# Optimization experiments

Measured on AMD Instinct MI355X. Metric: run time of the kernel, lower is better.

Reference implementation:

```python
import jax, jax.numpy as jnp
import numpy as np

B, T, D = 2, 2048, 1024
H, DK, DV, M = 4, 256, 256, 256  # heads, head_k_dim, head_v_dim, num_slots
GATE_NORM = 8.0
SCALE = 1.0
EPS = 1e-5


def setup_inputs() -> dict:
    key = jax.random.key(0)
    ks = jax.random.split(key, 7)
    w = lambda k, shp: jax.random.normal(k, shp, dtype=jnp.float32) * 0.02
    return {
        "hidden_states": jax.random.normal(ks[0], (B, T, D), dtype=jnp.float32),
        "Wq": w(ks[1], (H * DK, D)),   # q_proj
        "Wk": w(ks[2], (H * DK, D)),   # k_proj (num_kv_groups == 1)
        "Wv": w(ks[3], (H * DV, D)),   # v_proj
        "Wf": w(ks[4], (H * M, D)),    # f_proj (num_kv_heads * num_slots)
        "g_w": jnp.ones((H * DV,), dtype=jnp.float32),  # RMSNorm weight
        "Wo": w(ks[5], (D, H * DV)),   # o_proj
    }


def _gsa(q, k, v, s, f, scale):
    """Two-pass GLA recurrence (GSA). All inputs time-major [T,B,H,*]."""
    Bb, Hh = q.shape[1], q.shape[2]
    gk = jnp.exp(f)  # [T,B,H,M] decay in (0,1)

    # Pass 1: Hk_t = Hk_{t-1} * g_t (over slot dim) + k_t (x) s_t ; ok_t = q_t @ Hk_t
    def step1(S, inp):
        qt, kt, st, gt = inp
        S = S * gt[..., None, :] + kt[..., :, None] * st[..., None, :]
        return S, jnp.einsum('bhk,bhkm->bhm', qt * scale, S)

    S0k = jnp.zeros((Bb, Hh, DK, M), q.dtype)
    _, ok = jax.lax.scan(step1, S0k, (q, k, s, gk))

    qv = jax.nn.softmax(ok, axis=-1)  # [T,B,H,M]

    # Pass 2: Hv_t = Hv_{t-1} * g_t (over slot dim) + s_t (x) v_t ; o_t = qv_t @ Hv_t
    def step2(S, inp):
        qt, st, vt, gt = inp
        S = S * gt[..., :, None] + st[..., :, None] * vt[..., None, :]
        return S, jnp.einsum('bhm,bhmv->bhv', qt, S)

    S0v = jnp.zeros((Bb, Hh, M, DV), q.dtype)
    _, ov = jax.lax.scan(step2, S0v, (qv, s, v, gk))
    return ov  # [T,B,H,DV]


def reference(hidden_states, Wq, Wk, Wv, Wf, g_w, Wo):
    Bb, Tt, Dd = hidden_states.shape
    q = (hidden_states @ Wq.T).reshape(Bb, Tt, H, DK)
    k = (hidden_states @ Wk.T).reshape(Bb, Tt, H, DK)
    v = (hidden_states @ Wv.T).reshape(Bb, Tt, H, DV)
    f = (hidden_states @ Wf.T).reshape(Bb, Tt, H, M)

    q = jax.nn.silu(q)            # swish feature map
    k = jax.nn.silu(k)
    v = jax.nn.silu(v)
    f = jax.nn.log_sigmoid(f) / GATE_NORM   # forget-gate log decay
    s = 1.0 - jnp.exp(f)                     # slot write strength

    tm = lambda x: jnp.transpose(x, (1, 0, 2, 3))  # -> time-major
    ov = _gsa(tm(q), tm(k), tm(v), tm(s), tm(f), SCALE)
    o = jnp.transpose(ov, (1, 0, 2, 3)).reshape(Bb, Tt, H * DV)

    # rms_norm_linear(silu(o), g_norm.weight, None, Wo, None), norm in fp32
    o = jax.nn.silu(o)
    o32 = o.astype(jnp.float32)
    rms = o32 * jax.lax.rsqrt(jnp.mean(o32 * o32, axis=-1, keepdims=True) + EPS)
    return (rms * g_w).astype(hidden_states.dtype) @ Wo.T
```

## Files before the change

### kernel.cpp

```cpp
#include <hip/hip_runtime.h>
#include <math.h>

#define TLEN 2048
#define NROWS 4096
#define CHK 64
#define NCHK 32

typedef unsigned short u16;
typedef unsigned int u32;
typedef __attribute__((ext_vector_type(8))) short bf16x8;
typedef __attribute__((ext_vector_type(4))) float f32x4;

#define MFMA(a, b, c) __builtin_amdgcn_mfma_f32_16x16x32_bf16(a, b, c, 0, 0, 0)

__device__ __forceinline__ float bf2f(u16 u) {
    u32 v = ((u32)u) << 16; float f; __builtin_memcpy(&f, &v, 4); return f;
}
__device__ __forceinline__ u16 f2bf(float x) {
    u32 u; __builtin_memcpy(&u, &x, 4);
    u += 0x7FFFu + ((u >> 16) & 1u);
    return (u16)(u >> 16);
}
__device__ __forceinline__ u32 pack2bf(float a, float b) {
    return (u32)f2bf(a) | ((u32)f2bf(b) << 16);
}
__device__ __forceinline__ float bflo(u32 u) { return bf2f((u16)(u & 0xFFFFu)); }
__device__ __forceinline__ float bfhi(u32 u) { return bf2f((u16)(u >> 16)); }
__device__ __forceinline__ float siluf(float x) { return x / (1.f + expf(-x)); }

__global__ void gsa_detect(const u32* __restrict__ gw, int* __restrict__ flag) {
    *flag = (gw[0] == 0x3F803F80u) ? 1 : 0;
}

__global__ __launch_bounds__(256) void gsa_tobf16(const void* __restrict__ src,
        u16* __restrict__ dst, int n8, const int* __restrict__ flag) {
    int i = blockIdx.x * 256 + threadIdx.x;
    if (i >= n8) return;
    if (*flag) {
        ((uint4*)dst)[i] = ((const uint4*)src)[i];
    } else {
        float4 a = ((const float4*)src)[2 * i];
        float4 b = ((const float4*)src)[2 * i + 1];
        uint4 o;
        o.x = pack2bf(a.x, a.y); o.y = pack2bf(a.z, a.w);
        o.z = pack2bf(b.x, b.y); o.w = pack2bf(b.z, b.w);
        ((uint4*)dst)[i] = o;
    }
}

__global__ __launch_bounds__(256) void gsa_emit(const float* __restrict__ src,
        void* __restrict__ dst, int n4, const int* __restrict__ flag) {
    int i = blockIdx.x * 256 + threadIdx.x;
    if (i >= n4) return;
    float4 v = ((const float4*)src)[i];
    if (*flag) {
        uint2 u; u.x = pack2bf(v.x, v.y); u.y = pack2bf(v.z, v.w);
        ((uint2*)dst)[i] = u;
    } else {
        ((float4*)dst)[i] = v;
    }
}

#define GLOAD_LDS16(g, l) \
    __builtin_amdgcn_global_load_lds((const __attribute__((address_space(1))) void*)(g), \
                                     (__attribute__((address_space(3))) void*)(l), 16, 0, 0)

__global__ __launch_bounds__(256) void gsa_gemm_mfma(const u16* __restrict__ A,
        const u16* __restrict__ W0, const u16* __restrict__ W1,
        const u16* __restrict__ W2, const u16* __restrict__ W3,
        void* __restrict__ O0, void* __restrict__ O1,
        void* __restrict__ O2, void* __restrict__ O3, int actpack, int obfmask) {
    __shared__ u16 As[128 * 32];
    __shared__ u16 Bs[128 * 32];
    int tid = threadIdx.x;
    int sel = blockIdx.x >> 3;
    int ntile = blockIdx.x & 7;
    int mtile = blockIdx.y;
    const u16* W = (sel == 0) ? W0 : (sel == 1) ? W1 : (sel == 2) ? W2 : W3;
    void* Out    = (sel == 0) ? O0 : (sel == 1) ? O1 : (sel == 2) ? O2 : O3;
    int act = (actpack >> (sel * 8)) & 0xff;
    int obf = (obfmask >> sel) & 1;
    int w = tid >> 6, lane = tid & 63;
    int wm = w >> 1, wn = w & 1;
    int m0 = wm * 64, n0 = wn * 64;
    int srow = w * 32 + (lane >> 2);
    int scol = (lane & 3) * 8;
    const u16* Abase = A + (size_t)(mtile * 128 + srow) * 1024 + scol;
    const u16* Wbase = W + (size_t)(ntile * 128 + srow) * 1024 + scol;
    u16* AsDst0 = &As[(w * 32) * 32];
    u16* BsDst0 = &Bs[(w * 32) * 32];
    f32x4 acc[4][4];
    #pragma unroll
    for (int i = 0; i < 4; i++)
        #pragma unroll
        for (int j = 0; j < 4; j++) acc[i][j] = (f32x4){0.f, 0.f, 0.f, 0.f};
    int frow = lane & 15, fq = lane >> 4;
    for (int k0 = 0; k0 < 1024; k0 += 32) {
        __syncthreads();
        GLOAD_LDS16(Abase + k0, AsDst0);
        GLOAD_LDS16(Abase + k0 + (size_t)16 * 1024, AsDst0 + 16 * 32);
        GLOAD_LDS16(Wbase + k0, BsDst0);
        GLOAD_LDS16(Wbase + k0 + (size_t)16 * 1024, BsDst0 + 16 * 32);
        __syncthreads();
        bf16x8 af[4], bfv[4];
        #pragma unroll
        for (int mt = 0; mt < 4; mt++)
            af[mt] = *(const bf16x8*)&As[(m0 + mt * 16 + frow) * 32 + fq * 8];
        #pragma unroll
        for (int nt = 0; nt < 4; nt++)
            bfv[nt] = *(const bf16x8*)&Bs[(n0 + nt * 16 + frow) * 32 + fq * 8];
        #pragma unroll
        for (int mt = 0; mt < 4; mt++)
            #pragma unroll
            for (int nt = 0; nt < 4; nt++)
                acc[mt][nt] = MFMA(af[mt], bfv[nt], acc[mt][nt]);
    }
    #pragma unroll
    for (int mt = 0; mt < 4; mt++) {
        #pragma unroll
        for (int nt = 0; nt < 4; nt++) {
            #pragma unroll
            for (int r = 0; r < 4; r++) {
                float x = acc[mt][nt][r];
                int grow = mtile * 128 + m0 + mt * 16 + fq * 4 + r;
                int gcol = ntile * 128 + n0 + nt * 16 + frow;
                float val;
                if (act == 0) val = siluf(x);
                else if (act == 1) {
                    float ls = (x >= 0.f) ? -log1pf(expf(-x)) : (x - log1pf(expf(x)));
                    val = expf(0.125f * ls);
                } else val = x;
                size_t o = (size_t)grow * 1024 + gcol;
                if (obf) ((u16*)Out)[o] = f2bf(val);
                else     ((float*)Out)[o] = val;
            }
        }
    }
}

template<int P>
__global__ __launch_bounds__(256) void gsa_p_local(const u16* __restrict__ Xb,
        const float* __restrict__ GKp, u16* __restrict__ Sb, float* __restrict__ ECb) {
    __shared__ u16 Xt[256 * 72];
    __shared__ u16 Wt[256 * 72];
    int tid = threadIdx.x;
    int bh = blockIdx.x & 7, c = blockIdx.x >> 3;
    int b = bh >> 2, h = bh & 3, t0 = c * CHK;
    size_t gbase = ((size_t)(b * TLEN + t0)) * 1024 + h * 256;
    {
        const u16* xp = Xb + gbase + tid;
        #pragma unroll
        for (int t8 = 0; t8 < 8; t8++) {
            bf16x8 v;
            #pragma unroll
            for (int j = 0; j < 8; j++) v[j] = (short)xp[(size_t)(t8 * 8 + j) * 1024];
            *(bf16x8*)&Xt[tid * 72 + t8 * 8] = v;
        }
    }
    {
        float g[CHK], f[CHK];
        const float* gp = GKp + gbase + tid;
        #pragma unroll
        for (int t = 0; t < CHK; t++) g[t] = gp[(size_t)t * 1024];
        float phiC = 0.f;
        #pragma unroll
        for (int t = 0; t < CHK; t++) { f[t] = __logf(g[t]); phiC += f[t]; }
        if (P == 1) ECb[(bh * NCHK + c) * 256 + tid] = __expf(phiC);
        float phi = 0.f;
        #pragma unroll
        for (int t8 = 0; t8 < 8; t8++) {
            bf16x8 v;
            #pragma unroll
            for (int j = 0; j < 8; j++) {
                phi += f[t8 * 8 + j];
                v[j] = (short)f2bf((1.f - g[t8 * 8 + j]) * __expf(phiC - phi));
            }
            *(bf16x8*)&Wt[tid * 72 + t8 * 8] = v;
        }
    }
    __syncthreads();
    int w = tid >> 6, lane = tid & 63, frow = lane & 15, fq = lane >> 4;
    const u16* Arows = (P == 1) ? Wt : Xt;
    const u16* Brows = (P == 1) ? Xt : Wt;
    bf16x8 afr[4][2];
    #pragma unroll
    for (int it = 0; it < 4; it++)
        #pragma unroll
        for (int ks = 0; ks < 2; ks++)
            afr[it][ks] = *(const bf16x8*)&Arows[(w * 64 + it * 16 + frow) * 72 + ks * 32 + fq * 8];
    u16* Sp = Sb + (size_t)(bh * NCHK + c) * 65536;
    for (int jt = 0; jt < 16; jt++) {
        f32x4 ac[4];
        #pragma unroll
        for (int it = 0; it < 4; it++) ac[it] = (f32x4){0.f, 0.f, 0.f, 0.f};
        #pragma unroll
        for (int ks = 0; ks < 2; ks++) {
            bf16x8 bfr = *(const bf16x8*)&Brows[(jt * 16 + frow) * 72 + ks * 32 + fq * 8];
            #pragma unroll
            for (int it = 0; it < 4; it++) ac[it] = MFMA(afr[it][ks], bfr, ac[it]);
        }
        #pragma unroll
        for (int it = 0; it < 4; it++)
            #pragma unroll
            for (int r = 0; r < 4; r++)
                Sp[(size_t)(w * 64 + it * 16 + fq * 4 + r) * 256 + jt * 16 + frow]
                    = f2bf(ac[it][r]);
    }
}

__global__ __launch_bounds__(256) void gsa_scan1(u16* __restrict__ Sb,
        const float* __restrict__ ECb) {
    int bh = blockIdx.x & 7, part = blockIdx.x >> 3;
    int lin = part * 1024 + threadIdx.x * 4;
    int m = lin >> 8, k = lin & 255;
    u16* Sp = Sb + (size_t)bh * NCHK * 65536 + m * 256 + k;
    const float* Ep = ECb + bh * NCHK * 256 + m;
    float s0 = 0.f, s1 = 0.f, s2 = 0.f, s3 = 0.f;
    for (int c = 0; c < NCHK; c++) {
        uint2 d = *(uint2*)(Sp + (size_t)c * 65536);
        float ec = Ep[c * 256];
        uint2 o; o.x = pack2bf(s0, s1); o.y = pack2bf(s2, s3);
        *(uint2*)(Sp + (size_t)c * 65536) = o;
        s0 = fmaf(ec, s0, bflo(d.x)); s1 = fmaf(ec, s1, bfhi(d.x));
        s2 = fmaf(ec, s2, bflo(d.y)); s3 = fmaf(ec, s3, bfhi(d.y));
    }
}
__global__ __launch_bounds__(256) void gsa_scan2(u16* __restrict__ Sb,
        const float* __restrict__ ECb) {
    int bh = blockIdx.x & 7, part = blockIdx.x >> 3;
    int lin = part * 1024 + threadIdx.x * 4;
    int v = lin >> 8, m = lin & 255;
    u16* Sp = Sb + (size_t)bh * NCHK * 65536 + v * 256 + m;
    const float* Ep = ECb + bh * NCHK * 256 + m;
    float s0 = 0.f, s1 = 0.f, s2 = 0.f, s3 = 0.f;
    for (int c = 0; c < NCHK; c++) {
        uint2 d = *(uint2*)(Sp + (size_t)c * 65536);
        float4 e = *(const float4*)(Ep + c * 256);
        uint2 o; o.x = pack2bf(s0, s1); o.y = pack2bf(s2, s3);
        *(uint2*)(Sp + (size_t)c * 65536) = o;
        s0 = fmaf(e.x, s0, bflo(d.x)); s1 = fmaf(e.y, s1, bfhi(d.x));
        s2 = fmaf(e.z, s2, bflo(d.y)); s3 = fmaf(e.w, s3, bfhi(d.y));
    }
}

__global__ __launch_bounds__(256) void gsa_p1_out(const u16* __restrict__ Qb,
        const u16* __restrict__ Kb, const float* __restrict__ GKp,
        const u16* __restrict__ Sb, float* __restrict__ OK) {
    __shared__ u16 Qs[64 * 264];
    __shared__ float Asc[64 * 68];
    __shared__ float Gs[64 * 260];
    int tid = threadIdx.x;
    int bh = blockIdx.x & 7, c = blockIdx.x >> 3;
    int b = bh >> 2, h = bh & 3, t0 = c * CHK;
    size_t gbase = ((size_t)(b * TLEN + t0)) * 1024 + h * 256;
    #pragma unroll
    for (int j = 0; j < 8; j++) {
        int lin = j * 256 + tid;
        int t = lin >> 5, kg = (lin & 31) * 8;
        *(bf16x8*)&Qs[t * 264 + kg] = *(const bf16x8*)(Qb + gbase + (size_t)t * 1024 + kg);
    }
    __syncthreads();
    int w = tid >> 6, lane = tid & 63, frow = lane & 15, fq = lane >> 4;
    {
        const u16* Kg = Kb + gbase;
        #pragma unroll
        for (int tt = 0; tt < 4; tt++) {
            f32x4 ac = (f32x4){0.f, 0.f, 0.f, 0.f};
            #pragma unroll
            for (int ks = 0; ks < 8; ks++) {
                bf16x8 a = *(const bf16x8*)&Qs[(w * 16 + frow) * 264 + ks * 32 + fq * 8];
                bf16x8 bb = *(const bf16x8*)(Kg + (size_t)(tt * 16 + frow) * 1024 + ks * 32 + fq * 8);
                ac = MFMA(a, bb, ac);
            }
            #pragma unroll
            for (int r = 0; r < 4; r++) {
                int t = w * 16 + fq * 4 + r, tau = tt * 16 + frow;
                Asc[t * 68 + tau] = (tau <= t) ? ac[r] : 0.f;
            }
        }
    }
    {
        const u16* Sg = Sb + (size_t)(bh * NCHK + c) * 65536;
        f32x4 gac[4][4];
        #pragma unroll
        for (int tt = 0; tt < 4; tt++)
            #pragma unroll
            for (int mt = 0; mt < 4; mt++) gac[tt][mt] = (f32x4){0.f, 0.f, 0.f, 0.f};
        for (int ks = 0; ks < 8; ks++) {
            bf16x8 bfr[4], afr[4];
            #pragma unroll
            for (int mt = 0; mt < 4; mt++)
                bfr[mt] = *(const bf16x8*)(Sg + (size_t)(w * 64 + mt * 16 + frow) * 256 + ks * 32 + fq * 8);
            #pragma unroll
            for (int tt = 0; tt < 4; tt++)
                afr[tt] = *(const bf16x8*)&Qs[(tt * 16 + frow) * 264 + ks * 32 + fq * 8];
            #pragma unroll
            for (int tt = 0; tt < 4; tt++)
                #pragma unroll
                for (int mt = 0; mt < 4; mt++)
                    gac[tt][mt] = MFMA(afr[tt], bfr[mt], gac[tt][mt]);
        }
        #pragma unroll
        for (int tt = 0; tt < 4; tt++)
            #pragma unroll
            for (int mt = 0; mt < 4; mt++)
                #pragma unroll
                for (int r = 0; r < 4; r++)
                    Gs[(tt * 16 + fq * 4 + r) * 260 + w * 64 + mt * 16 + frow] = gac[tt][mt][r];
    }
    __syncthreads();
    float E[CHK], U[CHK];
    {
        float g[CHK];
        const float* gp = GKp + gbase + tid;
        #pragma unroll
        for (int t = 0; t < CHK; t++) g[t] = gp[(size_t)t * 1024];
        float phi = 0.f;
        #pragma unroll
        for (int t = 0; t < CHK; t++) {
            float f = __logf(g[t]); phi += f;
            E[t] = __expf(phi);
            U[t] = (1.f - g[t]) * __expf(-phi);
        }
    }
    float* okp = OK + gbase + tid;
    #pragma unroll
    for (int t = 0; t < CHK; t++) {
        float acc = 0.f;
        const int NG = (t < 32) ? 8 : 16;
        #pragma unroll
        for (int j = 0; j < NG; j++) {
            float4 a4 = *(const float4*)&Asc[t * 68 + j * 4];
            acc = fmaf(a4.x, U[4 * j + 0], acc);
            acc = fmaf(a4.y, U[4 * j + 1], acc);
            acc = fmaf(a4.z, U[4 * j + 2], acc);
            acc = fmaf(a4.w, U[4 * j + 3], acc);
        }
        okp[(size_t)t * 1024] = E[t] * (Gs[t * 260 + tid] + acc);
    }
}

__global__ __launch_bounds__(256) void gsa_softmax(float* __restrict__ x) {
    int row = blockIdx.x * 4 + (threadIdx.x >> 6);
    int lane = threadIdx.x & 63;
    float* p = x + (size_t)row * 256 + lane * 4;
    float4 v = *(float4*)p;
    float mx = fmaxf(fmaxf(v.x, v.y), fmaxf(v.z, v.w));
    #pragma unroll
    for (int off = 32; off; off >>= 1) mx = fmaxf(mx, __shfl_xor(mx, off));
    v.x = expf(v.x - mx); v.y = expf(v.y - mx);
    v.z = expf(v.z - mx); v.w = expf(v.w - mx);
    float sm = v.x + v.y + v.z + v.w;
    #pragma unroll
    for (int off = 32; off; off >>= 1) sm += __shfl_xor(sm, off);
    float inv = 1.f / sm;
    v.x *= inv; v.y *= inv; v.z *= inv; v.w *= inv;
    *(float4*)p = v;
}

__global__ __launch_bounds__(256) void gsa_p2_out(const float* __restrict__ QV,
        const u16* __restrict__ Vb, const float* __restrict__ GKp,
        const u16* __restrict__ Sb, float* __restrict__ OV) {
    __shared__ u16 qe[64 * 264];
    __shared__ u16 Us[64 * 264];
    __shared__ float Bsc[64 * 68];
    __shared__ float Gs[64 * 260];
    int tid = threadIdx.x;
    int bh = blockIdx.x & 7, c = blockIdx.x >> 3;
    int b = bh >> 2, h = bh & 3, t0 = c * CHK;
    size_t gbase = ((size_t)(b * TLEN + t0)) * 1024 + h * 256;
    {
        float g[CHK], qv[CHK];
        const float* gp = GKp + gbase + tid;
        const float* qp = QV + gbase + tid;
        #pragma unroll
        for (int t = 0; t < CHK; t++) g[t] = gp[(size_t)t * 1024];
        #pragma unroll
        for (int t = 0; t < CHK; t++) qv[t] = qp[(size_t)t * 1024];
        float phi = 0.f;
        #pragma unroll
        for (int t = 0; t < CHK; t++) {
            float f = __logf(g[t]); phi += f;
            float E = __expf(phi);
            qe[t * 264 + tid] = f2bf(qv[t] * E);
            Us[t * 264 + tid] = f2bf((1.f - g[t]) * __expf(-phi));
        }
    }
    __syncthreads();
    int w = tid >> 6, lane = tid & 63, frow = lane & 15, fq = lane >> 4;
    {
        const u16* Sg = Sb + (size_t)(bh * NCHK + c) * 65536;
        f32x4 gac[4][4];
        #pragma unroll
        for (int tt = 0; tt < 4; tt++)
            #pragma unroll
            for (int vt = 0; vt < 4; vt++) gac[tt][vt] = (f32x4){0.f, 0.f, 0.f, 0.f};
        for (int ks = 0; ks < 8; ks++) {
            bf16x8 bfr[4], afr[4];
            #pragma unroll
            for (int vt = 0; vt < 4; vt++)
                bfr[vt] = *(const bf16x8*)(Sg + (size_t)(w * 64 + vt * 16 + frow) * 256 + ks * 32 + fq * 8);
            #pragma unroll
            for (int tt = 0; tt < 4; tt++)
                afr[tt] = *(const bf16x8*)&qe[(tt * 16 + frow) * 264 + ks * 32 + fq * 8];
            #pragma unroll
            for (int tt = 0; tt < 4; tt++)
                #pragma unroll
                for (int vt = 0; vt < 4; vt++)
                    gac[tt][vt] = MFMA(afr[tt], bfr[vt], gac[tt][vt]);
        }
        #pragma unroll
        for (int tt = 0; tt < 4; tt++)
            #pragma unroll
            for (int vt = 0; vt < 4; vt++)
                #pragma unroll
                for (int r = 0; r < 4; r++)
                    Gs[(tt * 16 + fq * 4 + r) * 260 + w * 64 + vt * 16 + frow] = gac[tt][vt][r];
    }
    {
        #pragma unroll
        for (int tt = 0; tt < 4; tt++) {
            f32x4 ac = (f32x4){0.f, 0.f, 0.f, 0.f};
            #pragma unroll
            for (int ks = 0; ks < 8; ks++) {
                bf16x8 a = *(const bf16x8*)&qe[(w * 16 + frow) * 264 + ks * 32 + fq * 8];
                bf16x8 bb = *(const bf16x8*)&Us[(tt * 16 + frow) * 264 + ks * 32 + fq * 8];
                ac = MFMA(a, bb, ac);
            }
            #pragma unroll
            for (int r = 0; r < 4; r++) {
                int t = w * 16 + fq * 4 + r, tau = tt * 16 + frow;
                Bsc[t * 68 + tau] = (tau <= t) ? ac[r] : 0.f;
            }
        }
    }
    __syncthreads();
    float vcol[CHK];
    {
        const u16* vp = Vb + gbase + tid;
        #pragma unroll
        for (int t = 0; t < CHK; t++) vcol[t] = bf2f(vp[(size_t)t * 1024]);
    }
    float* ovp = OV + gbase + tid;
    #pragma unroll
    for (int t = 0; t < CHK; t++) {
        float acc = 0.f;
        const int NG = (t < 32) ? 8 : 16;
        #pragma unroll
        for (int j = 0; j < NG; j++) {
            float4 a4 = *(const float4*)&Bsc[t * 68 + j * 4];
            acc = fmaf(a4.x, vcol[4 * j + 0], acc);
            acc = fmaf(a4.y, vcol[4 * j + 1], acc);
            acc = fmaf(a4.z, vcol[4 * j + 2], acc);
            acc = fmaf(a4.w, vcol[4 * j + 3], acc);
        }
        ovp[(size_t)t * 1024] = Gs[t * 260 + tid] + acc;
    }
}

__global__ __launch_bounds__(256) void gsa_rmsnorm(const float* __restrict__ ov,
        const void* __restrict__ gw, const int* __restrict__ flag,
        u16* __restrict__ out) {
    __shared__ float part[4];
    int row = blockIdx.x;
    int tid = threadIdx.x;
    const float* p = ov + (size_t)row * 1024 + tid * 4;
    float4 x = *(const float4*)p;
    float y0 = siluf(x.x), y1 = siluf(x.y), y2 = siluf(x.z), y3 = siluf(x.w);
    float ssum = y0 * y0 + y1 * y1 + y2 * y2 + y3 * y3;
    #pragma unroll
    for (int off = 32; off; off >>= 1) ssum += __shfl_xor(ssum, off);
    if ((tid & 63) == 0) part[tid >> 6] = ssum;
    __syncthreads();
    float tot = part[0] + part[1] + part[2] + part[3];
    float r = rsqrtf(tot * (1.f / 1024.f) + 1e-5f);
    float4 g;
    if (*flag) {
        ushort4 u = ((const ushort4*)gw)[tid];
        g.x = bf2f(u.x); g.y = bf2f(u.y); g.z = bf2f(u.z); g.w = bf2f(u.w);
    } else {
        g = ((const float4*)gw)[tid];
    }
    ushort4 o;
    o.x = f2bf(y0 * r * g.x); o.y = f2bf(y1 * r * g.y);
    o.z = f2bf(y2 * r * g.z); o.w = f2bf(y3 * r * g.w);
    ((ushort4*)(out + (size_t)row * 1024))[tid] = o;
}

extern "C" void kernel_launch(void* const* d_in, const int* in_sizes, int n_in,
                              void* d_out, int out_size, void* d_ws, size_t ws_size,
                              hipStream_t stream) {
    (void)in_sizes; (void)n_in; (void)out_size; (void)ws_size;
    const void* hs_raw = d_in[0];
    const void* wq_raw = d_in[1];
    const void* wk_raw = d_in[2];
    const void* wv_raw = d_in[3];
    const void* wf_raw = d_in[4];
    const void* gw_raw = d_in[5];
    const void* wo_raw = d_in[6];

    char* base = (char*)d_ws;
    int* flag = (int*)base;
    float* fb = (float*)(base + 256);
    const size_t F1M = 1048576;
    u16* Qb   = (u16*)fb;
    u16* Kb   = (u16*)(fb + 2 * F1M);
    u16* Vb   = (u16*)(fb + 4 * F1M);
    float* GK = fb + 6 * F1M;
    float* OK = fb + 10 * F1M;
    u16* Sbuf = (u16*)(fb + 14 * F1M);
    float* ECb = fb + 14 * F1M + 8388608;
    u16* Wb   = (u16*)(fb + 14 * F1M + 8388608 + 65536);
    u16* WQb = Wb;
    u16* WKb = Wb + 1048576;
    u16* WVb = Wb + 2 * 1048576;
    u16* WFb = Wb + 3 * 1048576;
    u16* WOb = Wb + 4 * 1048576;
    u16* HSb  = (u16*)OK;
    float* OV = fb;
    u16* AN   = (u16*)OK;
    float* FO = GK;

    gsa_detect<<<1, 1, 0, stream>>>((const u32*)gw_raw, flag);
    gsa_tobf16<<<2048, 256, 0, stream>>>(hs_raw, HSb, 524288, flag);
    gsa_tobf16<<<512, 256, 0, stream>>>(wq_raw, WQb, 131072, flag);
    gsa_tobf16<<<512, 256, 0, stream>>>(wk_raw, WKb, 131072, flag);
    gsa_tobf16<<<512, 256, 0, stream>>>(wv_raw, WVb, 131072, flag);
    gsa_tobf16<<<512, 256, 0, stream>>>(wf_raw, WFb, 131072, flag);
    gsa_tobf16<<<512, 256, 0, stream>>>(wo_raw, WOb, 131072, flag);

    gsa_gemm_mfma<<<dim3(32, 32), 256, 0, stream>>>(HSb, WQb, WKb, WVb, WFb,
            Qb, Kb, Vb, GK, 0x01000000, 0x7);

    gsa_p_local<1><<<256, 256, 0, stream>>>(Kb, GK, Sbuf, ECb);
    gsa_scan1<<<512, 256, 0, stream>>>(Sbuf, ECb);
    gsa_p1_out<<<256, 256, 0, stream>>>(Qb, Kb, GK, Sbuf, OK);
    gsa_softmax<<<4096, 256, 0, stream>>>(OK);
    gsa_p_local<2><<<256, 256, 0, stream>>>(Vb, GK, Sbuf, ECb);
    gsa_scan2<<<512, 256, 0, stream>>>(Sbuf, ECb);
    gsa_p2_out<<<256, 256, 0, stream>>>(OK, Vb, GK, Sbuf, OV);

    gsa_rmsnorm<<<4096, 256, 0, stream>>>(OV, gw_raw, flag, AN);
    gsa_gemm_mfma<<<dim3(8, 32), 256, 0, stream>>>(AN, WOb, WOb, WOb, WOb,
            FO, FO, FO, FO, 0x02020202, 0x0);
    gsa_emit<<<4096, 256, 0, stream>>>(FO, d_out, 1048576, flag);
}
```

Measured before the change: 465.1 us.

## Load GEMM fragments directly from global memory with register double-buffering

The MFMA GEMM no longer stages A and W tiles through LDS with global_load_lds and two barriers per k-step. Each wave now loads its bf16x8 fragments straight from global memory into registers, double-buffered across two 32-wide k slices so the next loads overlap the current MFMAs. This removes the LDS traffic and block-wide synchronisation. In exchange, fragments that were shared through LDS are now fetched redundantly by each wave (every A row by both N-waves, every W row by both M-waves), relying on L1/L2 hits, and register pressure goes up.

```diff
diff --git a/kernel.cpp b/kernel.cpp
--- a/kernel.cpp
+++ b/kernel.cpp
@@ -61,17 +61,11 @@
     }
 }
 
-#define GLOAD_LDS16(g, l) \
-    __builtin_amdgcn_global_load_lds((const __attribute__((address_space(1))) void*)(g), \
-                                     (__attribute__((address_space(3))) void*)(l), 16, 0, 0)
-
-__global__ __launch_bounds__(256) void gsa_gemm_mfma(const u16* __restrict__ A,
+__global__ __launch_bounds__(256) void gsa_gemm_direct(const u16* __restrict__ A,
         const u16* __restrict__ W0, const u16* __restrict__ W1,
         const u16* __restrict__ W2, const u16* __restrict__ W3,
         void* __restrict__ O0, void* __restrict__ O1,
         void* __restrict__ O2, void* __restrict__ O3, int actpack, int obfmask) {
-    __shared__ u16 As[128 * 32];
-    __shared__ u16 Bs[128 * 32];
     int tid = threadIdx.x;
     int sel = blockIdx.x >> 3;
     int ntile = blockIdx.x & 7;
@@ -82,38 +76,49 @@
     int obf = (obfmask >> sel) & 1;
     int w = tid >> 6, lane = tid & 63;
     int wm = w >> 1, wn = w & 1;
-    int m0 = wm * 64, n0 = wn * 64;
-    int srow = w * 32 + (lane >> 2);
-    int scol = (lane & 3) * 8;
-    const u16* Abase = A + (size_t)(mtile * 128 + srow) * 1024 + scol;
-    const u16* Wbase = W + (size_t)(ntile * 128 + srow) * 1024 + scol;
-    u16* AsDst0 = &As[(w * 32) * 32];
-    u16* BsDst0 = &Bs[(w * 32) * 32];
+    int frow = lane & 15, fq = lane >> 4;
+    const u16* Ap[4];
+    const u16* Bp[4];
+    #pragma unroll
+    for (int i = 0; i < 4; i++) {
+        Ap[i] = A + (size_t)(mtile * 128 + wm * 64 + i * 16 + frow) * 1024 + fq * 8;
+        Bp[i] = W + (size_t)(ntile * 128 + wn * 64 + i * 16 + frow) * 1024 + fq * 8;
+    }
     f32x4 acc[4][4];
     #pragma unroll
     for (int i = 0; i < 4; i++)
         #pragma unroll
         for (int j = 0; j < 4; j++) acc[i][j] = (f32x4){0.f, 0.f, 0.f, 0.f};
-    int frow = lane & 15, fq = lane >> 4;
-    for (int k0 = 0; k0 < 1024; k0 += 32) {
-        __syncthreads();
-        GLOAD_LDS16(Abase + k0, AsDst0);
-        GLOAD_LDS16(Abase + k0 + (size_t)16 * 1024, AsDst0 + 16 * 32);
-        GLOAD_LDS16(Wbase + k0, BsDst0);
-        GLOAD_LDS16(Wbase + k0 + (size_t)16 * 1024, BsDst0 + 16 * 32);
-        __syncthreads();
-        bf16x8 af[4], bfv[4];
+
+    bf16x8 afA[4], bfA[4], afB[4], bfB[4];
+    #pragma unroll
+    for (int i = 0; i < 4; i++) {
+        afA[i] = *(const bf16x8*)(Ap[i]);
+        bfA[i] = *(const bf16x8*)(Bp[i]);
+    }
+    for (int k0 = 0; k0 < 1024; k0 += 64) {
+        #pragma unroll
+        for (int i = 0; i < 4; i++) {
+            afB[i] = *(const bf16x8*)(Ap[i] + k0 + 32);
+            bfB[i] = *(const bf16x8*)(Bp[i] + k0 + 32);
+        }
         #pragma unroll
         for (int mt = 0; mt < 4; mt++)
-            af[mt] = *(const bf16x8*)&As[(m0 + mt * 16 + frow) * 32 + fq * 8];
-        #pragma unroll
-        for (int nt = 0; nt < 4; nt++)
-            bfv[nt] = *(const bf16x8*)&Bs[(n0 + nt * 16 + frow) * 32 + fq * 8];
+            #pragma unroll
+            for (int nt = 0; nt < 4; nt++)
+                acc[mt][nt] = MFMA(afA[mt], bfA[nt], acc[mt][nt]);
+        if (k0 + 64 < 1024) {
+            #pragma unroll
+            for (int i = 0; i < 4; i++) {
+                afA[i] = *(const bf16x8*)(Ap[i] + k0 + 64);
+                bfA[i] = *(const bf16x8*)(Bp[i] + k0 + 64);
+            }
+        }
         #pragma unroll
         for (int mt = 0; mt < 4; mt++)
             #pragma unroll
             for (int nt = 0; nt < 4; nt++)
-                acc[mt][nt] = MFMA(af[mt], bfv[nt], acc[mt][nt]);
+                acc[mt][nt] = MFMA(afB[mt], bfB[nt], acc[mt][nt]);
     }
     #pragma unroll
     for (int mt = 0; mt < 4; mt++) {
@@ -122,8 +127,8 @@
             #pragma unroll
             for (int r = 0; r < 4; r++) {
                 float x = acc[mt][nt][r];
-                int grow = mtile * 128 + m0 + mt * 16 + fq * 4 + r;
-                int gcol = ntile * 128 + n0 + nt * 16 + frow;
+                int grow = mtile * 128 + wm * 64 + mt * 16 + fq * 4 + r;
+                int gcol = ntile * 128 + wn * 64 + nt * 16 + frow;
                 float val;
                 if (act == 0) val = siluf(x);
                 else if (act == 1) {
@@ -529,7 +534,7 @@
     gsa_tobf16<<<512, 256, 0, stream>>>(wf_raw, WFb, 131072, flag);
     gsa_tobf16<<<512, 256, 0, stream>>>(wo_raw, WOb, 131072, flag);
 
-    gsa_gemm_mfma<<<dim3(32, 32), 256, 0, stream>>>(HSb, WQb, WKb, WVb, WFb,
+    gsa_gemm_direct<<<dim3(32, 32), 256, 0, stream>>>(HSb, WQb, WKb, WVb, WFb,
             Qb, Kb, Vb, GK, 0x01000000, 0x7);
 
     gsa_p_local<1><<<256, 256, 0, stream>>>(Kb, GK, Sbuf, ECb);
@@ -541,7 +546,7 @@
     gsa_p2_out<<<256, 256, 0, stream>>>(OK, Vb, GK, Sbuf, OV);
 
     gsa_rmsnorm<<<4096, 256, 0, stream>>>(OV, gw_raw, flag, AN);
-    gsa_gemm_mfma<<<dim3(8, 32), 256, 0, stream>>>(AN, WOb, WOb, WOb, WOb,
+    gsa_gemm_direct<<<dim3(8, 32), 256, 0, stream>>>(AN, WOb, WOb, WOb, WOb,
             FO, FO, FO, FO, 0x02020202, 0x0);
     gsa_emit<<<4096, 256, 0, stream>>>(FO, d_out, 1048576, flag);
 }
```

Measured after the change: 513.5 us. +10.4%, slower.
